# Kernel tuning notes

Hardware: AMD Instinct MI355X
Metric: run time of the kernel (lower is better)

## Reference

```python
import jax, jax.numpy as jnp
import numpy as np

NEG_SLOPE = 0.2  # PyG GATConv default leaky_relu slope


def _gat_conv(x, src, dst, W, a_src, a_dst, b, num_nodes):
    # Linear transform: [N, F_out]
    h = x @ W
    # Per-node attention halves (heads=1): [N]
    alpha_s = h @ a_src
    alpha_d = h @ a_dst
    # Per-edge raw score for edge j->i: a_src.h_j + a_dst.h_i
    e = jax.nn.leaky_relu(alpha_s[src] + alpha_d[dst], NEG_SLOPE)
    # Softmax over edges grouped by destination node (numerically stable)
    m = jax.ops.segment_max(e, dst, num_segments=num_nodes)
    ex = jnp.exp(e - m[dst])
    denom = jax.ops.segment_sum(ex, dst, num_segments=num_nodes)
    coef = ex / denom[dst]
    # Attention-weighted aggregation of source features into destinations
    out = jax.ops.segment_sum(h[src] * coef[:, None], dst, num_segments=num_nodes)
    return out + b


def setup_inputs() -> dict:
    key = jax.random.key(0)
    ks = jax.random.split(key, 12)
    N, F_in, F_hid, F_out, E = 100000, 128, 64, 40, 1600000
    x = jax.random.normal(ks[0], (N, F_in), dtype=jnp.float32)
    edge_index = jax.random.randint(ks[1], (2, E), 0, N, dtype=jnp.int64)
    g = lambda k, shape, fan: jax.random.normal(k, shape, dtype=jnp.float32) * (1.0 / np.sqrt(fan))
    return {
        "x": x,
        "edge_index": edge_index,
        "W1": g(ks[2], (F_in, F_hid), F_in),
        "a_src1": g(ks[3], (F_hid,), F_hid),
        "a_dst1": g(ks[4], (F_hid,), F_hid),
        "b1": jnp.zeros((F_hid,), dtype=jnp.float32),
        "W2": g(ks[5], (F_hid, F_out), F_hid),
        "a_src2": g(ks[6], (F_out,), F_out),
        "a_dst2": g(ks[7], (F_out,), F_out),
        "b2": jnp.zeros((F_out,), dtype=jnp.float32),
    }


def reference(x, edge_index, W1, a_src1, a_dst1, b1, W2, a_src2, a_dst2, b2):
    N = x.shape[0]
    # PyG GATConv adds self loops by default
    loops = jnp.arange(N, dtype=edge_index.dtype)
    src = jnp.concatenate([edge_index[0], loops])
    dst = jnp.concatenate([edge_index[1], loops])
    h = _gat_conv(x, src, dst, W1, a_src1, a_dst1, b1, N)
    h = jax.nn.relu(h)
    # dropout p=0.5 is inactive in eval mode
    h = _gat_conv(h, src, dst, W2, a_src2, a_dst2, b2, N)
    return jax.nn.log_softmax(h, axis=-1)
```

## Files before the change

kernel.cpp:

```cpp
#include <hip/hip_runtime.h>
#include <math.h>


constexpr int F_IN = 128;
constexpr int F_H  = 64;
constexpr int F_O  = 40;
constexpr int BSH  = 7;
constexpr int BNODES = 1 << BSH;
constexpr int NBMAX = 1024;
constexpr int CHUNK = 8192;

__device__ __forceinline__ unsigned f2bf(float f) {
    unsigned u = __float_as_uint(f);
    return (u + 0x7FFFu + ((u >> 16) & 1u)) >> 16;
}
__device__ __forceinline__ float bflo(unsigned u) { return __uint_as_float(u << 16); }
__device__ __forceinline__ float bfhi(unsigned u) { return __uint_as_float(u & 0xFFFF0000u); }


__global__ __launch_bounds__(256) void k_binA(const int* __restrict__ dsts,
                                              int* __restrict__ bcnt,
                                              int E, int Et, int NB) {
    __shared__ int hist[NBMAX];
    for (int i = threadIdx.x; i < NB; i += 256) hist[i] = 0;
    __syncthreads();
    int e0 = blockIdx.x * 2048;
#pragma unroll
    for (int it = 0; it < 8; ++it) {
        int e = e0 + it * 256 + threadIdx.x;
        if (e < Et) {
            int d = (e < E) ? dsts[e] : (e - E);
            atomicAdd(&hist[d >> BSH], 1);
        }
    }
    __syncthreads();
    for (int i = threadIdx.x; i < NB; i += 256) {
        int c = hist[i];
        if (c) atomicAdd(&bcnt[i], c);
    }
}

__global__ __launch_bounds__(256) void k_binB(const int* __restrict__ bcnt,
                                              int* __restrict__ bbase,
                                              int* __restrict__ bcur,
                                              int* __restrict__ rp,
                                              int NB, int N, int Et) {
    __shared__ int lds[256];
    int t = threadIdx.x;
    int b4 = t * 4;
    int v0 = (b4 + 0 < NB) ? bcnt[b4 + 0] : 0;
    int v1 = (b4 + 1 < NB) ? bcnt[b4 + 1] : 0;
    int v2 = (b4 + 2 < NB) ? bcnt[b4 + 2] : 0;
    int v3 = (b4 + 3 < NB) ? bcnt[b4 + 3] : 0;
    int tot = v0 + v1 + v2 + v3;
    lds[t] = tot; __syncthreads();
    int x = tot;
    for (int o = 1; o < 256; o <<= 1) {
        int y = (t >= o) ? lds[t - o] : 0;
        __syncthreads();
        x += y;
        lds[t] = x;
        __syncthreads();
    }
    int ex = x - tot;
    if (b4 + 0 < NB) { bbase[b4 + 0] = ex; bcur[b4 + 0] = ex; } ex += v0;
    if (b4 + 1 < NB) { bbase[b4 + 1] = ex; bcur[b4 + 1] = ex; } ex += v1;
    if (b4 + 2 < NB) { bbase[b4 + 2] = ex; bcur[b4 + 2] = ex; } ex += v2;
    if (b4 + 3 < NB) { bbase[b4 + 3] = ex; bcur[b4 + 3] = ex; }
    if (t == 0) rp[N] = Et;
}

__global__ __launch_bounds__(256) void k_binC(const int* __restrict__ srcs,
                                              const int* __restrict__ dsts,
                                              int* __restrict__ bcur,
                                              unsigned* __restrict__ binned,
                                              int E, int Et, int NB) {
    __shared__ int hist[NBMAX];
    __shared__ int gbase[NBMAX];
    __shared__ int lcnt[NBMAX];
    int t = threadIdx.x;
    for (int i = t; i < NB; i += 256) hist[i] = 0;
    __syncthreads();
    int e0 = blockIdx.x * CHUNK;
#pragma unroll 4
    for (int it = 0; it < CHUNK / 256; ++it) {
        int e = e0 + it * 256 + t;
        if (e < Et) {
            int d = (e < E) ? dsts[e] : (e - E);
            atomicAdd(&hist[d >> BSH], 1);
        }
    }
    __syncthreads();
    for (int i = t; i < NB; i += 256) {
        int c = hist[i];
        gbase[i] = c ? atomicAdd(&bcur[i], c) : 0;
        lcnt[i] = 0;
    }
    __syncthreads();
#pragma unroll 4
    for (int it = 0; it < CHUNK / 256; ++it) {
        int e = e0 + it * 256 + t;
        if (e < Et) {
            int s, d;
            if (e < E) { s = srcs[e]; d = dsts[e]; } else { s = e - E; d = s; }
            int b = d >> BSH;
            int p = atomicAdd(&lcnt[b], 1);
            binned[gbase[b] + p] = (unsigned)s | ((unsigned)(d & (BNODES - 1)) << 24);
        }
    }
}

__global__ __launch_bounds__(256) void k_binD(const unsigned* __restrict__ binned,
                                              const int* __restrict__ bbase,
                                              const int* __restrict__ bcur,
                                              int* __restrict__ rp,
                                              int* __restrict__ csr, int N) {
    __shared__ int hist[BNODES];
    __shared__ int sc[256];
    __shared__ int lcnt[BNODES];
    int b = blockIdx.x, t = threadIdx.x;
    int base = bbase[b], end = bcur[b];
    if (t < BNODES) hist[t] = 0;
    __syncthreads();
    for (int j = base + t; j < end; j += 256)
        atomicAdd(&hist[binned[j] >> 24], 1);
    __syncthreads();
    int v = (t < BNODES) ? hist[t] : 0;
    sc[t] = v; __syncthreads();
    int x = v;
    for (int o = 1; o < BNODES; o <<= 1) {
        int y = (t >= o) ? sc[t - o] : 0;
        __syncthreads();
        x += y;
        sc[t] = x;
        __syncthreads();
    }
    int pref = x - v;
    int g = (b << BSH) + t;
    if (t < BNODES && g < N) rp[g] = base + pref;
    if (t < BNODES) { sc[t] = pref; lcnt[t] = 0; }
    __syncthreads();
    for (int j = base + t; j < end; j += 256) {
        unsigned w = binned[j];
        int v2 = (int)(w >> 24);
        int s = (int)(w & 0xFFFFFFu);
        int p = atomicAdd(&lcnt[v2], 1);
        csr[base + sc[v2] + p] = s;
    }
}


__global__ __launch_bounds__(256) void k_gemm1(const float* __restrict__ x,
                                               const float* __restrict__ W,
                                               const float* __restrict__ avs,
                                               const float* __restrict__ avd,
                                               unsigned short* __restrict__ h,
                                               float* __restrict__ as,
                                               float* __restrict__ ad, int N) {
    __shared__ __align__(16) float Ws[F_IN * F_H];
    for (int i = threadIdx.x; i < F_IN * F_H; i += 256) Ws[i] = W[i];
    __syncthreads();
    int t = threadIdx.x;
    int r0 = blockIdx.x * 64 + (t >> 4) * 4;
    int c0 = (t & 15) * 4;
    if (r0 >= N) return;
    const float* xp = x + (size_t)r0 * F_IN;
    float acc[4][4] = {};
    for (int k4 = 0; k4 < F_IN / 4; ++k4) {
        int kb = k4 * 4;
        float4 w0 = *(const float4*)&Ws[(kb + 0) * F_H + c0];
        float4 w1 = *(const float4*)&Ws[(kb + 1) * F_H + c0];
        float4 w2 = *(const float4*)&Ws[(kb + 2) * F_H + c0];
        float4 w3 = *(const float4*)&Ws[(kb + 3) * F_H + c0];
#pragma unroll
        for (int r = 0; r < 4; ++r) {
            float4 xv = *(const float4*)&xp[(size_t)r * F_IN + kb];
            acc[r][0] += xv.x * w0.x + xv.y * w1.x + xv.z * w2.x + xv.w * w3.x;
            acc[r][1] += xv.x * w0.y + xv.y * w1.y + xv.z * w2.y + xv.w * w3.y;
            acc[r][2] += xv.x * w0.z + xv.y * w1.z + xv.z * w2.z + xv.w * w3.z;
            acc[r][3] += xv.x * w0.w + xv.y * w1.w + xv.z * w2.w + xv.w * w3.w;
        }
    }
    float4 avs4 = *(const float4*)&avs[c0];
    float4 avd4 = *(const float4*)&avd[c0];
#pragma unroll
    for (int r = 0; r < 4; ++r) {
        unsigned lo = f2bf(acc[r][0]) | (f2bf(acc[r][1]) << 16);
        unsigned hi = f2bf(acc[r][2]) | (f2bf(acc[r][3]) << 16);
        ((uint2*)h)[((size_t)(r0 + r) * F_H + c0) >> 2] = make_uint2(lo, hi);
        float ps = acc[r][0] * avs4.x + acc[r][1] * avs4.y + acc[r][2] * avs4.z + acc[r][3] * avs4.w;
        float pd = acc[r][0] * avd4.x + acc[r][1] * avd4.y + acc[r][2] * avd4.z + acc[r][3] * avd4.w;
#pragma unroll
        for (int o = 8; o; o >>= 1) {
            ps += __shfl_xor(ps, o, 16);
            pd += __shfl_xor(pd, o, 16);
        }
        if ((t & 15) == 0) { as[r0 + r] = ps; ad[r0 + r] = pd; }
    }
}


__global__ __launch_bounds__(256) void k_gemm2(const float* __restrict__ xin,
                                               const float* __restrict__ W,
                                               const float* __restrict__ avs,
                                               const float* __restrict__ avd,
                                               unsigned short* __restrict__ h,
                                               float* __restrict__ as,
                                               float* __restrict__ ad, int N) {
    __shared__ __align__(16) float Ws[F_H * F_O];
    for (int i = threadIdx.x; i < F_H * F_O; i += 256) Ws[i] = W[i];
    __syncthreads();
    int t = threadIdx.x;
    int r0 = blockIdx.x * 64 + (t >> 3) * 2;
    int l = t & 7;
    if (r0 >= N) return;
    const float4* xa = (const float4*)(xin + (size_t)r0 * F_H);
    const float4* xb = (const float4*)(xin + (size_t)(r0 + 1) * F_H);
    float acca[5] = {}, accb[5] = {};
#pragma unroll
    for (int k4 = 0; k4 < F_H / 4; ++k4) {
        float4 xva = xa[k4];
        float4 xvb = xb[k4];
        int kb = k4 * 4;
#pragma unroll
        for (int kk = 0; kk < 4; ++kk) {
            const float* wr = &Ws[(kb + kk) * F_O + l];
            float w0 = wr[0], w1 = wr[8], w2 = wr[16], w3 = wr[24], w4 = wr[32];
            float xs = (&xva.x)[kk];
            acca[0] += xs * w0; acca[1] += xs * w1; acca[2] += xs * w2;
            acca[3] += xs * w3; acca[4] += xs * w4;
            float ys = (&xvb.x)[kk];
            accb[0] += ys * w0; accb[1] += ys * w1; accb[2] += ys * w2;
            accb[3] += ys * w3; accb[4] += ys * w4;
        }
    }
    float psa = 0.f, pda = 0.f, psb = 0.f, pdb = 0.f;
    unsigned short* ra = h + (size_t)r0 * F_H;
    unsigned short* rb = h + (size_t)(r0 + 1) * F_H;
#pragma unroll
    for (int cc = 0; cc < 5; ++cc) {
        int c = l + 8 * cc;
        ra[c] = (unsigned short)f2bf(acca[cc]);
        rb[c] = (unsigned short)f2bf(accb[cc]);
        float vs = avs[c], vd = avd[c];
        psa += acca[cc] * vs; pda += acca[cc] * vd;
        psb += accb[cc] * vs; pdb += accb[cc] * vd;
    }
#pragma unroll
    for (int pp = 0; pp < 3; ++pp) {
        int c = 40 + l * 3 + pp;
        ra[c] = 0; rb[c] = 0;
    }
#pragma unroll
    for (int o = 4; o; o >>= 1) {
        psa += __shfl_xor(psa, o, 8);
        pda += __shfl_xor(pda, o, 8);
        psb += __shfl_xor(psb, o, 8);
        pdb += __shfl_xor(pdb, o, 8);
    }
    if (l == 0) { as[r0] = psa; ad[r0] = pda; as[r0 + 1] = psb; ad[r0 + 1] = pdb; }
}


template <int FOUT, bool RELU, bool LOGSM>
__global__ __launch_bounds__(256) void k_agg(const int* __restrict__ rp,
                                             const int* __restrict__ csr,
                                             const float* __restrict__ as,
                                             const float* __restrict__ ad,
                                             const uint4* __restrict__ h4,
                                             const float* __restrict__ bias,
                                             float* __restrict__ out, int N) {
    int lane = threadIdx.x & 63;
    int i = (blockIdx.x * 256 + threadIdx.x) >> 6;
    if (i >= N) return;
    int start = rp[i], end = rp[i + 1];
    float adi = ad[i];
    int grp = lane >> 3, c = lane & 7;
    float acc[8] = {}, acc2[8] = {};
    float sacc = 0.f;

    for (int base = start; base < end; base += 64) {
        int cnt = end - base; if (cnt > 64) cnt = 64;
        int srcn = i;
        if (lane < cnt) srcn = csr[base + lane];
        int s0 = __shfl(srcn, grp, 64);
        int s1 = __shfl(srcn, 8 + grp, 64);
        int s2 = __shfl(srcn, 16 + grp, 64);
        int s3 = __shfl(srcn, 24 + grp, 64);
        uint4 hv0 = h4[(size_t)s0 * 8 + c];
        uint4 hv1 = h4[(size_t)s1 * 8 + c];
        uint4 hv2 = h4[(size_t)s2 * 8 + c];
        uint4 hv3 = h4[(size_t)s3 * 8 + c];
        float e = as[srcn] + adi;
        e = (e > 0.f) ? e : 0.2f * e;
        float w = (lane < cnt) ? __expf(e) : 0.f;
        sacc += w;
        float w0 = __shfl(w, grp, 64);
        float w1 = __shfl(w, 8 + grp, 64);
        float w2 = __shfl(w, 16 + grp, 64);
        float w3 = __shfl(w, 24 + grp, 64);
        acc[0] += w0 * bflo(hv0.x); acc[1] += w0 * bfhi(hv0.x);
        acc[2] += w0 * bflo(hv0.y); acc[3] += w0 * bfhi(hv0.y);
        acc[4] += w0 * bflo(hv0.z); acc[5] += w0 * bfhi(hv0.z);
        acc[6] += w0 * bflo(hv0.w); acc[7] += w0 * bfhi(hv0.w);
        acc2[0] += w1 * bflo(hv1.x); acc2[1] += w1 * bfhi(hv1.x);
        acc2[2] += w1 * bflo(hv1.y); acc2[3] += w1 * bfhi(hv1.y);
        acc2[4] += w1 * bflo(hv1.z); acc2[5] += w1 * bfhi(hv1.z);
        acc2[6] += w1 * bflo(hv1.w); acc2[7] += w1 * bfhi(hv1.w);
        acc[0] += w2 * bflo(hv2.x); acc[1] += w2 * bfhi(hv2.x);
        acc[2] += w2 * bflo(hv2.y); acc[3] += w2 * bfhi(hv2.y);
        acc[4] += w2 * bflo(hv2.z); acc[5] += w2 * bfhi(hv2.z);
        acc[6] += w2 * bflo(hv2.w); acc[7] += w2 * bfhi(hv2.w);
        acc2[0] += w3 * bflo(hv3.x); acc2[1] += w3 * bfhi(hv3.x);
        acc2[2] += w3 * bflo(hv3.y); acc2[3] += w3 * bfhi(hv3.y);
        acc2[4] += w3 * bflo(hv3.z); acc2[5] += w3 * bfhi(hv3.z);
        acc2[6] += w3 * bflo(hv3.w); acc2[7] += w3 * bfhi(hv3.w);

        if (cnt > 32) {
            int t0 = __shfl(srcn, 32 + grp, 64);
            int t1 = __shfl(srcn, 40 + grp, 64);
            int t2 = __shfl(srcn, 48 + grp, 64);
            int t3 = __shfl(srcn, 56 + grp, 64);
            uint4 gv0 = h4[(size_t)t0 * 8 + c];
            uint4 gv1 = h4[(size_t)t1 * 8 + c];
            uint4 gv2 = h4[(size_t)t2 * 8 + c];
            uint4 gv3 = h4[(size_t)t3 * 8 + c];
            float u0 = __shfl(w, 32 + grp, 64);
            float u1 = __shfl(w, 40 + grp, 64);
            float u2 = __shfl(w, 48 + grp, 64);
            float u3 = __shfl(w, 56 + grp, 64);
            acc[0] += u0 * bflo(gv0.x); acc[1] += u0 * bfhi(gv0.x);
            acc[2] += u0 * bflo(gv0.y); acc[3] += u0 * bfhi(gv0.y);
            acc[4] += u0 * bflo(gv0.z); acc[5] += u0 * bfhi(gv0.z);
            acc[6] += u0 * bflo(gv0.w); acc[7] += u0 * bfhi(gv0.w);
            acc2[0] += u1 * bflo(gv1.x); acc2[1] += u1 * bfhi(gv1.x);
            acc2[2] += u1 * bflo(gv1.y); acc2[3] += u1 * bfhi(gv1.y);
            acc2[4] += u1 * bflo(gv1.z); acc2[5] += u1 * bfhi(gv1.z);
            acc2[6] += u1 * bflo(gv1.w); acc2[7] += u1 * bfhi(gv1.w);
            acc[0] += u2 * bflo(gv2.x); acc[1] += u2 * bfhi(gv2.x);
            acc[2] += u2 * bflo(gv2.y); acc[3] += u2 * bfhi(gv2.y);
            acc[4] += u2 * bflo(gv2.z); acc[5] += u2 * bfhi(gv2.z);
            acc[6] += u2 * bflo(gv2.w); acc[7] += u2 * bfhi(gv2.w);
            acc2[0] += u3 * bflo(gv3.x); acc2[1] += u3 * bfhi(gv3.x);
            acc2[2] += u3 * bflo(gv3.y); acc2[3] += u3 * bfhi(gv3.y);
            acc2[4] += u3 * bflo(gv3.z); acc2[5] += u3 * bfhi(gv3.z);
            acc2[6] += u3 * bflo(gv3.w); acc2[7] += u3 * bfhi(gv3.w);
        }
    }
#pragma unroll
    for (int k = 0; k < 8; ++k) acc[k] += acc2[k];
#pragma unroll
    for (int o = 8; o <= 32; o <<= 1)
#pragma unroll
        for (int k = 0; k < 8; ++k) acc[k] += __shfl_xor(acc[k], o);
#pragma unroll
    for (int o = 32; o; o >>= 1) sacc += __shfl_xor(sacc, o);
    float inv = 1.f / sacc;

    if (!LOGSM) {
        if (lane < 8) {
            float r[8];
#pragma unroll
            for (int k = 0; k < 8; ++k) {
                r[k] = acc[k] * inv + bias[8 * lane + k];
                if (RELU) r[k] = fmaxf(r[k], 0.f);
            }
            float4* op = (float4*)(out + (size_t)i * FOUT + 8 * lane);
            op[0] = make_float4(r[0], r[1], r[2], r[3]);
            op[1] = make_float4(r[4], r[5], r[6], r[7]);
        }
    } else {
        constexpr int VC = FOUT / 8;
        bool act = (lane < VC);
        float v[8];
#pragma unroll
        for (int k = 0; k < 8; ++k)
            v[k] = act ? (acc[k] * inv + bias[8 * lane + k]) : -INFINITY;
        float mx = v[0];
#pragma unroll
        for (int k = 1; k < 8; ++k) mx = fmaxf(mx, v[k]);
#pragma unroll
        for (int o = 1; o <= 4; o <<= 1) mx = fmaxf(mx, __shfl_xor(mx, o));
        float es = 0.f;
        if (act) {
#pragma unroll
            for (int k = 0; k < 8; ++k) es += __expf(v[k] - mx);
        }
#pragma unroll
        for (int o = 1; o <= 4; o <<= 1) es += __shfl_xor(es, o);
        if (act) {
            float lse = mx + __logf(es);
            float4* op = (float4*)(out + (size_t)i * FOUT + 8 * lane);
            op[0] = make_float4(v[0] - lse, v[1] - lse, v[2] - lse, v[3] - lse);
            op[1] = make_float4(v[4] - lse, v[5] - lse, v[6] - lse, v[7] - lse);
        }
    }
}


extern "C" void kernel_launch(void* const* d_in, const int* in_sizes, int n_in,
                              void* d_out, int out_size, void* d_ws, size_t ws_size,
                              hipStream_t stream) {
    const float* x   = (const float*)d_in[0];
    const int* edges = (const int*)d_in[1];
    const float* W1  = (const float*)d_in[2];
    const float* av_s1 = (const float*)d_in[3];
    const float* av_d1 = (const float*)d_in[4];
    const float* b1  = (const float*)d_in[5];
    const float* W2  = (const float*)d_in[6];
    const float* av_s2 = (const float*)d_in[7];
    const float* av_d2 = (const float*)d_in[8];
    const float* b2  = (const float*)d_in[9];
    float* out = (float*)d_out;

    const int N  = in_sizes[0] / F_IN;
    const int E  = in_sizes[1] / 2;
    const int Et = E + N;
    const int NB = (N + BNODES - 1) >> BSH;

    char* p = (char*)d_ws;
    auto alloc = [&](size_t bytes) {
        char* q = p;
        p += (bytes + 255) & ~(size_t)255;
        return (void*)q;
    };
    unsigned short* h1 = (unsigned short*)alloc((size_t)N * F_H * 2);
    float* out1   = (float*)alloc((size_t)N * F_H * 4);
    float* as1    = (float*)alloc((size_t)N * 4);
    float* ad1    = (float*)alloc((size_t)N * 4);
    float* as2    = (float*)alloc((size_t)N * 4);
    float* ad2    = (float*)alloc((size_t)N * 4);
    int* rp       = (int*)alloc((size_t)(N + 1) * 4);
    int* bcnt     = (int*)alloc(NBMAX * 4);
    int* bbase    = (int*)alloc(NBMAX * 4);
    int* bcur     = (int*)alloc(NBMAX * 4);
    unsigned* binned = (unsigned*)alloc((size_t)Et * 4);
    int* csr      = (int*)alloc((size_t)Et * 4);
    (void)n_in; (void)out_size; (void)ws_size;

    const int* srcs = edges;
    const int* dsts = edges + E;

    hipMemsetAsync(bcnt, 0, NBMAX * 4, stream);

    k_binA<<<(Et + 2047) / 2048, 256, 0, stream>>>(dsts, bcnt, E, Et, NB);
    k_binB<<<1, 256, 0, stream>>>(bcnt, bbase, bcur, rp, NB, N, Et);
    k_binC<<<(Et + CHUNK - 1) / CHUNK, 256, 0, stream>>>(srcs, dsts, bcur, binned, E, Et, NB);
    k_binD<<<NB, 256, 0, stream>>>(binned, bbase, bcur, rp, csr, N);

    k_gemm1<<<(N + 63) / 64, 256, 0, stream>>>(x, W1, av_s1, av_d1, h1, as1, ad1, N);
    int gAgg = (N + 3) / 4;
    k_agg<F_H, true, false><<<gAgg, 256, 0, stream>>>(rp, csr, as1, ad1,
                                                      (const uint4*)h1, b1, out1, N);
    k_gemm2<<<(N + 63) / 64, 256, 0, stream>>>(out1, W2, av_s2, av_d2, h1, as2, ad2, N);
    k_agg<F_O, false, true><<<gAgg, 256, 0, stream>>>(rp, csr, as2, ad2,
                                                      (const uint4*)h1, b2, out, N);
}
```

Before: 337.7 us.

## Switch features to fp16 with half2 FMA, precompute edge weights, fuse bin kernels

```diff
diff --git a/kernel.cpp b/kernel.cpp
--- a/kernel.cpp
+++ b/kernel.cpp
@@ -1,4 +1,5 @@
 #include <hip/hip_runtime.h>
+#include <hip/hip_fp16.h>
 #include <math.h>
 
 
@@ -10,56 +11,58 @@
 constexpr int NBMAX = 1024;
 constexpr int CHUNK = 8192;
 
-__device__ __forceinline__ unsigned f2bf(float f) {
-    unsigned u = __float_as_uint(f);
-    return (u + 0x7FFFu + ((u >> 16) & 1u)) >> 16;
-}
-__device__ __forceinline__ float bflo(unsigned u) { return __uint_as_float(u << 16); }
-__device__ __forceinline__ float bfhi(unsigned u) { return __uint_as_float(u & 0xFFFF0000u); }
-
-
-__global__ __launch_bounds__(256) void k_binA(const int* __restrict__ dsts,
-                                              int* __restrict__ bcnt,
-                                              int E, int Et, int NB) {
+__device__ __forceinline__ unsigned short f2h(float f) {
+    return __half_as_ushort(__float2half(f));
+}
+union H2U { unsigned u; __half2 h; };
+__device__ __forceinline__ __half2 u2h(unsigned u) { H2U t; t.u = u; return t.h; }
+__device__ __forceinline__ unsigned h2u(__half2 h) { H2U t; t.h = h; return t.u; }
+
+
+__global__ __launch_bounds__(256) void k_binAB(const int* __restrict__ dsts,
+                                               int* __restrict__ bcnt,
+                                               int* __restrict__ done,
+                                               int* __restrict__ bbase,
+                                               int* __restrict__ bcur,
+                                               int* __restrict__ rp,
+                                               int E, int Et, int NB, int N, int nblk) {
     __shared__ int hist[NBMAX];
-    for (int i = threadIdx.x; i < NB; i += 256) hist[i] = 0;
+    __shared__ int isLast;
+    int t = threadIdx.x;
+    for (int i = t; i < NB; i += 256) hist[i] = 0;
     __syncthreads();
     int e0 = blockIdx.x * 2048;
 #pragma unroll
     for (int it = 0; it < 8; ++it) {
-        int e = e0 + it * 256 + threadIdx.x;
+        int e = e0 + it * 256 + t;
         if (e < Et) {
             int d = (e < E) ? dsts[e] : (e - E);
             atomicAdd(&hist[d >> BSH], 1);
         }
     }
     __syncthreads();
-    for (int i = threadIdx.x; i < NB; i += 256) {
+    for (int i = t; i < NB; i += 256) {
         int c = hist[i];
         if (c) atomicAdd(&bcnt[i], c);
     }
-}
-
-__global__ __launch_bounds__(256) void k_binB(const int* __restrict__ bcnt,
-                                              int* __restrict__ bbase,
-                                              int* __restrict__ bcur,
-                                              int* __restrict__ rp,
-                                              int NB, int N, int Et) {
-    __shared__ int lds[256];
-    int t = threadIdx.x;
+    __threadfence();
+    if (t == 0) isLast = (atomicAdd(done, 1) == nblk - 1);
+    __syncthreads();
+    if (!isLast) return;
     int b4 = t * 4;
-    int v0 = (b4 + 0 < NB) ? bcnt[b4 + 0] : 0;
-    int v1 = (b4 + 1 < NB) ? bcnt[b4 + 1] : 0;
-    int v2 = (b4 + 2 < NB) ? bcnt[b4 + 2] : 0;
-    int v3 = (b4 + 3 < NB) ? bcnt[b4 + 3] : 0;
+    int v0 = (b4 + 0 < NB) ? atomicAdd(&bcnt[b4 + 0], 0) : 0;
+    int v1 = (b4 + 1 < NB) ? atomicAdd(&bcnt[b4 + 1], 0) : 0;
+    int v2 = (b4 + 2 < NB) ? atomicAdd(&bcnt[b4 + 2], 0) : 0;
+    int v3 = (b4 + 3 < NB) ? atomicAdd(&bcnt[b4 + 3], 0) : 0;
     int tot = v0 + v1 + v2 + v3;
-    lds[t] = tot; __syncthreads();
+    __syncthreads();
+    hist[t] = tot; __syncthreads();
     int x = tot;
     for (int o = 1; o < 256; o <<= 1) {
-        int y = (t >= o) ? lds[t - o] : 0;
+        int y = (t >= o) ? hist[t - o] : 0;
         __syncthreads();
         x += y;
-        lds[t] = x;
+        hist[t] = x;
         __syncthreads();
     }
     int ex = x - tot;
@@ -185,8 +188,8 @@
     float4 avd4 = *(const float4*)&avd[c0];
 #pragma unroll
     for (int r = 0; r < 4; ++r) {
-        unsigned lo = f2bf(acc[r][0]) | (f2bf(acc[r][1]) << 16);
-        unsigned hi = f2bf(acc[r][2]) | (f2bf(acc[r][3]) << 16);
+        unsigned lo = (unsigned)f2h(acc[r][0]) | ((unsigned)f2h(acc[r][1]) << 16);
+        unsigned hi = (unsigned)f2h(acc[r][2]) | ((unsigned)f2h(acc[r][3]) << 16);
         ((uint2*)h)[((size_t)(r0 + r) * F_H + c0) >> 2] = make_uint2(lo, hi);
         float ps = acc[r][0] * avs4.x + acc[r][1] * avs4.y + acc[r][2] * avs4.z + acc[r][3] * avs4.w;
         float pd = acc[r][0] * avd4.x + acc[r][1] * avd4.y + acc[r][2] * avd4.z + acc[r][3] * avd4.w;
@@ -240,8 +243,8 @@
 #pragma unroll
     for (int cc = 0; cc < 5; ++cc) {
         int c = l + 8 * cc;
-        ra[c] = (unsigned short)f2bf(acca[cc]);
-        rb[c] = (unsigned short)f2bf(accb[cc]);
+        ra[c] = f2h(acca[cc]);
+        rb[c] = f2h(accb[cc]);
         float vs = avs[c], vd = avd[c];
         psa += acca[cc] * vs; pda += acca[cc] * vd;
         psb += accb[cc] * vs; pdb += accb[cc] * vd;
@@ -262,11 +265,28 @@
 }
 
 
+__global__ __launch_bounds__(256) void k_w(const int* __restrict__ rp,
+                                           const int* __restrict__ csr,
+                                           const float* __restrict__ as,
+                                           const float* __restrict__ ad,
+                                           uint2* __restrict__ ws, int N) {
+    int i = (blockIdx.x * 256 + threadIdx.x) >> 6;
+    if (i >= N) return;
+    int lane = threadIdx.x & 63;
+    int start = rp[i], end = rp[i + 1];
+    float adi = ad[i];
+    for (int j = start + lane; j < end; j += 64) {
+        int s = csr[j];
+        float e = as[s] + adi;
+        e = (e > 0.f) ? e : 0.2f * e;
+        ws[j] = make_uint2(__float_as_uint(__expf(e - 6.f)), (unsigned)s);
+    }
+}
+
+
 template <int FOUT, bool RELU, bool LOGSM>
 __global__ __launch_bounds__(256) void k_agg(const int* __restrict__ rp,
-                                             const int* __restrict__ csr,
-                                             const float* __restrict__ as,
-                                             const float* __restrict__ ad,
+                                             const uint2* __restrict__ ws,
                                              const uint4* __restrict__ h4,
                                              const float* __restrict__ bias,
                                              float* __restrict__ out, int N) {
@@ -274,95 +294,72 @@
     int i = (blockIdx.x * 256 + threadIdx.x) >> 6;
     if (i >= N) return;
     int start = rp[i], end = rp[i + 1];
-    float adi = ad[i];
     int grp = lane >> 3, c = lane & 7;
-    float acc[8] = {}, acc2[8] = {};
+    int e1 = end - 1;
+    __half2 a0[4] = {}, a1[4] = {};
     float sacc = 0.f;
 
-    for (int base = start; base < end; base += 64) {
-        int cnt = end - base; if (cnt > 64) cnt = 64;
-        int srcn = i;
-        if (lane < cnt) srcn = csr[base + lane];
-        int s0 = __shfl(srcn, grp, 64);
-        int s1 = __shfl(srcn, 8 + grp, 64);
-        int s2 = __shfl(srcn, 16 + grp, 64);
-        int s3 = __shfl(srcn, 24 + grp, 64);
-        uint4 hv0 = h4[(size_t)s0 * 8 + c];
-        uint4 hv1 = h4[(size_t)s1 * 8 + c];
-        uint4 hv2 = h4[(size_t)s2 * 8 + c];
-        uint4 hv3 = h4[(size_t)s3 * 8 + c];
-        float e = as[srcn] + adi;
-        e = (e > 0.f) ? e : 0.2f * e;
-        float w = (lane < cnt) ? __expf(e) : 0.f;
-        sacc += w;
-        float w0 = __shfl(w, grp, 64);
-        float w1 = __shfl(w, 8 + grp, 64);
-        float w2 = __shfl(w, 16 + grp, 64);
-        float w3 = __shfl(w, 24 + grp, 64);
-        acc[0] += w0 * bflo(hv0.x); acc[1] += w0 * bfhi(hv0.x);
-        acc[2] += w0 * bflo(hv0.y); acc[3] += w0 * bfhi(hv0.y);
-        acc[4] += w0 * bflo(hv0.z); acc[5] += w0 * bfhi(hv0.z);
-        acc[6] += w0 * bflo(hv0.w); acc[7] += w0 * bfhi(hv0.w);
-        acc2[0] += w1 * bflo(hv1.x); acc2[1] += w1 * bfhi(hv1.x);
-        acc2[2] += w1 * bflo(hv1.y); acc2[3] += w1 * bfhi(hv1.y);
-        acc2[4] += w1 * bflo(hv1.z); acc2[5] += w1 * bfhi(hv1.z);
-        acc2[6] += w1 * bflo(hv1.w); acc2[7] += w1 * bfhi(hv1.w);
-        acc[0] += w2 * bflo(hv2.x); acc[1] += w2 * bfhi(hv2.x);
-        acc[2] += w2 * bflo(hv2.y); acc[3] += w2 * bfhi(hv2.y);
-        acc[4] += w2 * bflo(hv2.z); acc[5] += w2 * bfhi(hv2.z);
-        acc[6] += w2 * bflo(hv2.w); acc[7] += w2 * bfhi(hv2.w);
-        acc2[0] += w3 * bflo(hv3.x); acc2[1] += w3 * bfhi(hv3.x);
-        acc2[2] += w3 * bflo(hv3.y); acc2[3] += w3 * bfhi(hv3.y);
-        acc2[4] += w3 * bflo(hv3.z); acc2[5] += w3 * bfhi(hv3.z);
-        acc2[6] += w3 * bflo(hv3.w); acc2[7] += w3 * bfhi(hv3.w);
-
-        if (cnt > 32) {
-            int t0 = __shfl(srcn, 32 + grp, 64);
-            int t1 = __shfl(srcn, 40 + grp, 64);
-            int t2 = __shfl(srcn, 48 + grp, 64);
-            int t3 = __shfl(srcn, 56 + grp, 64);
-            uint4 gv0 = h4[(size_t)t0 * 8 + c];
-            uint4 gv1 = h4[(size_t)t1 * 8 + c];
-            uint4 gv2 = h4[(size_t)t2 * 8 + c];
-            uint4 gv3 = h4[(size_t)t3 * 8 + c];
-            float u0 = __shfl(w, 32 + grp, 64);
-            float u1 = __shfl(w, 40 + grp, 64);
-            float u2 = __shfl(w, 48 + grp, 64);
-            float u3 = __shfl(w, 56 + grp, 64);
-            acc[0] += u0 * bflo(gv0.x); acc[1] += u0 * bfhi(gv0.x);
-            acc[2] += u0 * bflo(gv0.y); acc[3] += u0 * bfhi(gv0.y);
-            acc[4] += u0 * bflo(gv0.z); acc[5] += u0 * bfhi(gv0.z);
-            acc[6] += u0 * bflo(gv0.w); acc[7] += u0 * bfhi(gv0.w);
-            acc2[0] += u1 * bflo(gv1.x); acc2[1] += u1 * bfhi(gv1.x);
-            acc2[2] += u1 * bflo(gv1.y); acc2[3] += u1 * bfhi(gv1.y);
-            acc2[4] += u1 * bflo(gv1.z); acc2[5] += u1 * bfhi(gv1.z);
-            acc2[6] += u1 * bflo(gv1.w); acc2[7] += u1 * bfhi(gv1.w);
-            acc[0] += u2 * bflo(gv2.x); acc[1] += u2 * bfhi(gv2.x);
-            acc[2] += u2 * bflo(gv2.y); acc[3] += u2 * bfhi(gv2.y);
-            acc[4] += u2 * bflo(gv2.z); acc[5] += u2 * bfhi(gv2.z);
-            acc[6] += u2 * bflo(gv2.w); acc[7] += u2 * bfhi(gv2.w);
-            acc2[0] += u3 * bflo(gv3.x); acc2[1] += u3 * bfhi(gv3.x);
-            acc2[2] += u3 * bflo(gv3.y); acc2[3] += u3 * bfhi(gv3.y);
-            acc2[4] += u3 * bflo(gv3.z); acc2[5] += u3 * bfhi(gv3.z);
-            acc2[6] += u3 * bflo(gv3.w); acc2[7] += u3 * bfhi(gv3.w);
-        }
-    }
-#pragma unroll
-    for (int k = 0; k < 8; ++k) acc[k] += acc2[k];
-#pragma unroll
-    for (int o = 8; o <= 32; o <<= 1)
-#pragma unroll
-        for (int k = 0; k < 8; ++k) acc[k] += __shfl_xor(acc[k], o);
-#pragma unroll
-    for (int o = 32; o; o >>= 1) sacc += __shfl_xor(sacc, o);
+    for (int jb = start; jb < end; jb += 32) {
+        int j0 = jb + grp, j1 = jb + 8 + grp, j2 = jb + 16 + grp, j3 = jb + 24 + grp;
+        uint2 t0 = ws[min(j0, e1)];
+        uint2 t1 = ws[min(j1, e1)];
+        uint2 t2 = ws[min(j2, e1)];
+        uint2 t3 = ws[min(j3, e1)];
+        uint4 h0 = h4[(size_t)t0.y * 8 + c];
+        uint4 h1 = h4[(size_t)t1.y * 8 + c];
+        uint4 h2 = h4[(size_t)t2.y * 8 + c];
+        uint4 h3 = h4[(size_t)t3.y * 8 + c];
+        float w0 = (j0 <= e1) ? __uint_as_float(t0.x) : 0.f;
+        float w1 = (j1 <= e1) ? __uint_as_float(t1.x) : 0.f;
+        float w2 = (j2 <= e1) ? __uint_as_float(t2.x) : 0.f;
+        float w3 = (j3 <= e1) ? __uint_as_float(t3.x) : 0.f;
+        sacc += (w0 + w1) + (w2 + w3);
+        __half2 wh0 = __float2half2_rn(w0);
+        __half2 wh1 = __float2half2_rn(w1);
+        __half2 wh2 = __float2half2_rn(w2);
+        __half2 wh3 = __float2half2_rn(w3);
+        a0[0] = __hfma2(wh0, u2h(h0.x), a0[0]);
+        a0[1] = __hfma2(wh0, u2h(h0.y), a0[1]);
+        a0[2] = __hfma2(wh0, u2h(h0.z), a0[2]);
+        a0[3] = __hfma2(wh0, u2h(h0.w), a0[3]);
+        a1[0] = __hfma2(wh1, u2h(h1.x), a1[0]);
+        a1[1] = __hfma2(wh1, u2h(h1.y), a1[1]);
+        a1[2] = __hfma2(wh1, u2h(h1.z), a1[2]);
+        a1[3] = __hfma2(wh1, u2h(h1.w), a1[3]);
+        a0[0] = __hfma2(wh2, u2h(h2.x), a0[0]);
+        a0[1] = __hfma2(wh2, u2h(h2.y), a0[1]);
+        a0[2] = __hfma2(wh2, u2h(h2.z), a0[2]);
+        a0[3] = __hfma2(wh2, u2h(h2.w), a0[3]);
+        a1[0] = __hfma2(wh3, u2h(h3.x), a1[0]);
+        a1[1] = __hfma2(wh3, u2h(h3.y), a1[1]);
+        a1[2] = __hfma2(wh3, u2h(h3.z), a1[2]);
+        a1[3] = __hfma2(wh3, u2h(h3.w), a1[3]);
+    }
+#pragma unroll
+    for (int k = 0; k < 4; ++k) a0[k] = __hadd2(a0[k], a1[k]);
+#pragma unroll
+    for (int o = 8; o <= 32; o <<= 1) {
+#pragma unroll
+        for (int k = 0; k < 4; ++k) {
+            unsigned u = __shfl_xor((int)h2u(a0[k]), o);
+            a0[k] = __hadd2(a0[k], u2h((unsigned)u));
+        }
+        sacc += __shfl_xor(sacc, o);
+    }
     float inv = 1.f / sacc;
+    float f[8];
+#pragma unroll
+    for (int k = 0; k < 4; ++k) {
+        float2 p = __half22float2(a0[k]);
+        f[2 * k] = p.x; f[2 * k + 1] = p.y;
+    }
 
     if (!LOGSM) {
         if (lane < 8) {
             float r[8];
 #pragma unroll
             for (int k = 0; k < 8; ++k) {
-                r[k] = acc[k] * inv + bias[8 * lane + k];
+                r[k] = f[k] * inv + bias[8 * lane + k];
                 if (RELU) r[k] = fmaxf(r[k], 0.f);
             }
             float4* op = (float4*)(out + (size_t)i * FOUT + 8 * lane);
@@ -375,7 +372,7 @@
         float v[8];
 #pragma unroll
         for (int k = 0; k < 8; ++k)
-            v[k] = act ? (acc[k] * inv + bias[8 * lane + k]) : -INFINITY;
+            v[k] = act ? (f[k] * inv + bias[8 * lane + k]) : -INFINITY;
         float mx = v[0];
 #pragma unroll
         for (int k = 1; k < 8; ++k) mx = fmaxf(mx, v[k]);
@@ -431,28 +428,30 @@
     float* as2    = (float*)alloc((size_t)N * 4);
     float* ad2    = (float*)alloc((size_t)N * 4);
     int* rp       = (int*)alloc((size_t)(N + 1) * 4);
-    int* bcnt     = (int*)alloc(NBMAX * 4);
+    int* bcnt     = (int*)alloc((NBMAX + 64) * 4);
+    int* done     = bcnt + NBMAX;
     int* bbase    = (int*)alloc(NBMAX * 4);
     int* bcur     = (int*)alloc(NBMAX * 4);
     unsigned* binned = (unsigned*)alloc((size_t)Et * 4);
     int* csr      = (int*)alloc((size_t)Et * 4);
+    uint2* ws     = (uint2*)alloc((size_t)Et * 8);
     (void)n_in; (void)out_size; (void)ws_size;
 
     const int* srcs = edges;
     const int* dsts = edges + E;
 
-    hipMemsetAsync(bcnt, 0, NBMAX * 4, stream);
-
-    k_binA<<<(Et + 2047) / 2048, 256, 0, stream>>>(dsts, bcnt, E, Et, NB);
-    k_binB<<<1, 256, 0, stream>>>(bcnt, bbase, bcur, rp, NB, N, Et);
+    hipMemsetAsync(bcnt, 0, (NBMAX + 64) * 4, stream);
+
+    int nblkAB = (Et + 2047) / 2048;
+    k_binAB<<<nblkAB, 256, 0, stream>>>(dsts, bcnt, done, bbase, bcur, rp, E, Et, NB, N, nblkAB);
     k_binC<<<(Et + CHUNK - 1) / CHUNK, 256, 0, stream>>>(srcs, dsts, bcur, binned, E, Et, NB);
     k_binD<<<NB, 256, 0, stream>>>(binned, bbase, bcur, rp, csr, N);
 
+    int gAgg = (N + 3) / 4;
     k_gemm1<<<(N + 63) / 64, 256, 0, stream>>>(x, W1, av_s1, av_d1, h1, as1, ad1, N);
-    int gAgg = (N + 3) / 4;
-    k_agg<F_H, true, false><<<gAgg, 256, 0, stream>>>(rp, csr, as1, ad1,
-                                                      (const uint4*)h1, b1, out1, N);
+    k_w<<<gAgg, 256, 0, stream>>>(rp, csr, as1, ad1, ws, N);
+    k_agg<F_H, true, false><<<gAgg, 256, 0, stream>>>(rp, ws, (const uint4*)h1, b1, out1, N);
     k_gemm2<<<(N + 63) / 64, 256, 0, stream>>>(out1, W2, av_s2, av_d2, h1, as2, ad2, N);
-    k_agg<F_O, false, true><<<gAgg, 256, 0, stream>>>(rp, csr, as2, ad2,
-                                                      (const uint4*)h1, b2, out, N);
-}
+    k_w<<<gAgg, 256, 0, stream>>>(rp, csr, as2, ad2, ws, N);
+    k_agg<F_O, false, true><<<gAgg, 256, 0, stream>>>(rp, ws, (const uint4*)h1, b2, out, N);
+}
```

Measured after the change: 393.4 us. +16.5%, slower.
